# Performance work log

Measured on AMD Instinct MI355X. Metric: run time of the kernel, lower is better.

## Reference

```python
import jax, jax.numpy as jnp
import numpy as np


def _compact_positions(mask, K):
    """mask: [B, T] bool. Returns [B, K] with the (ascending) indices t where
    mask[b, t] is True, compacted to the front; remaining slots are -1.
    Stable argsort on ~mask puts True positions first, preserving order.
    """
    order = jnp.argsort(jnp.logical_not(mask), axis=1, stable=True)  # [B, T]
    counts = mask.sum(axis=1, keepdims=True)                          # [B, 1]
    pos = order[:, :K]                                                # [B, K]
    valid = jnp.arange(K)[None, :] < jnp.minimum(counts, K)
    return jnp.where(valid, pos, -1)


def setup_inputs() -> dict:
    key = jax.random.key(0)
    k_r, k_e = jax.random.split(key)
    B, MAX_ROUTING, D = 16, 4096, 512
    routing = jax.random.randint(k_r, (B, MAX_ROUTING), 0, 2, dtype=jnp.int32)
    pos_embed = jax.random.normal(k_e, (MAX_ROUTING, D), dtype=jnp.float32)
    return {"routing": routing, "max_nodes": 1024, "max_edges": 2048,
            "pos_embed": pos_embed}


def reference(routing, max_nodes, max_edges, pos_embed):
    # Compacted logical positions of node tokens (routing==0) and edge tokens
    # (routing==1), replacing the sequential per-batch Python loop.
    node_pos = _compact_positions(routing == 0, max_nodes)  # [B, max_nodes]
    edge_pos = _compact_positions(routing == 1, max_edges)  # [B, max_edges]

    # Each node spans 2 tokens, each edge spans 5 tokens:
    # unsqueeze(-1).repeat(...,k).view == elementwise repeat along axis 1.
    node_tok = jnp.repeat(node_pos, 2, axis=1)  # [B, max_nodes*2]
    edge_tok = jnp.repeat(edge_pos, 5, axis=1)  # [B, max_edges*5]

    node_pe = pos_embed[jnp.maximum(node_tok, 0)]  # [B, max_nodes*2, D]
    edge_pe = pos_embed[jnp.maximum(edge_tok, 0)]  # [B, max_edges*5, D]
    return node_pe, edge_pe
```

## Files before the change

kernel.cpp:

```cpp
#include <hip/hip_runtime.h>

#define NB 16
#define NT 4096
#define ND 512
#define ND4 128
#define MAX_NODES 1024
#define MAX_EDGES 2048
#define NODE_ROWS 2048
#define EDGE_ROWS 10240

__global__ __launch_bounds__(1024) void compact_kernel(
    const int* __restrict__ routing,
    int* __restrict__ node_pos,
    int* __restrict__ edge_pos)
{
    const int b   = blockIdx.x;
    const int tid = threadIdx.x;
    const int lane = tid & 63;
    const int wv   = tid >> 6;

    const int4 v = reinterpret_cast<const int4*>(routing + b * NT)[tid];
    const int e0 = v.x, e1 = v.y, e2 = v.z, e3 = v.w;

    unsigned inc0 = ((e0 == 0) ? 0x10000u : 0u) | ((e0 == 1) ? 1u : 0u);
    unsigned inc1 = ((e1 == 0) ? 0x10000u : 0u) | ((e1 == 1) ? 1u : 0u);
    unsigned inc2 = ((e2 == 0) ? 0x10000u : 0u) | ((e2 == 1) ? 1u : 0u);
    unsigned inc3 = ((e3 == 0) ? 0x10000u : 0u) | ((e3 == 1) ? 1u : 0u);
    unsigned p0 = inc0;
    unsigned p1 = p0 + inc1;
    unsigned p2 = p1 + inc2;
    unsigned p3 = p2 + inc3;
    const unsigned my_sum = p3;

    unsigned x = my_sum;
    #pragma unroll
    for (int off = 1; off < 64; off <<= 1) {
        unsigned y = __shfl_up(x, off, 64);
        if (lane >= off) x += y;
    }

    __shared__ unsigned wave_sums[16];
    if (lane == 63) wave_sums[wv] = x;

    node_pos[b * MAX_NODES + tid] = -1;
    edge_pos[b * MAX_EDGES + 2 * tid + 0] = -1;
    edge_pos[b * MAX_EDGES + 2 * tid + 1] = -1;
    __syncthreads();

    unsigned offset = 0;
    for (int i = 0; i < wv; ++i) offset += wave_sums[i];

    const unsigned base = offset + x - my_sum;

    const unsigned ex0 = base;
    const unsigned ex1 = base + p0;
    const unsigned ex2 = base + p1;
    const unsigned ex3 = base + p2;

    const int t0 = tid * 4;
    #pragma unroll 4
    for (int i = 0; i < 4; ++i) {
        const int      e  = (i == 0) ? e0 : (i == 1) ? e1 : (i == 2) ? e2 : e3;
        const unsigned ex = (i == 0) ? ex0 : (i == 1) ? ex1 : (i == 2) ? ex2 : ex3;
        if (e == 0) {
            const unsigned rank = ex >> 16;
            if (rank < MAX_NODES) node_pos[b * MAX_NODES + rank] = t0 + i;
        } else if (e == 1) {
            const unsigned rank = ex & 0xFFFFu;
            if (rank < MAX_EDGES) edge_pos[b * MAX_EDGES + rank] = t0 + i;
        }
    }
}

__global__ __launch_bounds__(256) void gather_node_kernel(
    const float4* __restrict__ pe,
    const int* __restrict__ node_pos,
    float4* __restrict__ out)
{
    const unsigned gid = blockIdx.x * 256u + threadIdx.x;
    const unsigned row = gid >> 7;
    const unsigned c   = gid & 127u;
    const unsigned b   = row >> 11;
    const unsigned j   = row & 2047u;
    const int tok = node_pos[b * MAX_NODES + (j >> 1)];
    const int src = tok < 0 ? 0 : tok;
    out[(size_t)row * ND4 + c] = pe[(size_t)src * ND4 + c];
}

__global__ __launch_bounds__(256) void gather_edge_kernel(
    const float4* __restrict__ pe,
    const int* __restrict__ edge_pos,
    float4* __restrict__ out)
{
    const unsigned gid = blockIdx.x * 256u + threadIdx.x;
    const unsigned row = gid >> 7;
    const unsigned c   = gid & 127u;
    const unsigned b   = row / EDGE_ROWS;
    const unsigned j   = row - b * EDGE_ROWS;
    const int tok = edge_pos[b * MAX_EDGES + j / 5u];
    const int src = tok < 0 ? 0 : tok;
    out[(size_t)row * ND4 + c] = pe[(size_t)src * ND4 + c];
}

extern "C" void kernel_launch(void* const* d_in, const int* in_sizes, int n_in,
                              void* d_out, int out_size, void* d_ws, size_t ws_size,
                              hipStream_t stream) {
    const int*   routing = (const int*)d_in[0];
    const float* pe      = (const float*)d_in[3];

    int* node_pos = (int*)d_ws;
    int* edge_pos = node_pos + NB * MAX_NODES;

    float* out_node = (float*)d_out;
    float* out_edge = out_node + (size_t)NB * NODE_ROWS * ND;

    compact_kernel<<<NB, 1024, 0, stream>>>(routing, node_pos, edge_pos);

    const unsigned node_threads = NB * NODE_ROWS * ND4;
    const unsigned edge_threads = NB * EDGE_ROWS * ND4;
    gather_node_kernel<<<node_threads / 256, 256, 0, stream>>>(
        (const float4*)pe, node_pos, (float4*)out_node);
    gather_edge_kernel<<<edge_threads / 256, 256, 0, stream>>>(
        (const float4*)pe, edge_pos, (float4*)out_edge);
}
```

Measured before the change: 428.5 us.

## Fuse node and edge gathers into one kernel with nontemporal stores

Merges the two gather kernels into a single launch covering all output rows, assigning 64 threads per row with each thread copying two float4s. Output writes use nontemporal stores so the large streaming output does not pollute cache. The intent is to remove one kernel launch and its tail, halve the index loads per row, and improve write streaming. The cost is a per-thread branch between the node and edge paths.

```diff
diff --git a/kernel.cpp b/kernel.cpp
--- a/kernel.cpp
+++ b/kernel.cpp
@@ -8,6 +8,10 @@
 #define MAX_EDGES 2048
 #define NODE_ROWS 2048
 #define EDGE_ROWS 10240
+#define ROWS_NODE_TOT 32768u
+#define ROWS_TOTAL 196608u
+
+typedef __attribute__((ext_vector_type(4))) float f4;
 
 __global__ __launch_bounds__(1024) void compact_kernel(
     const int* __restrict__ routing,
@@ -72,34 +76,36 @@
     }
 }
 
-__global__ __launch_bounds__(256) void gather_node_kernel(
+__global__ __launch_bounds__(256) void gather_fused_kernel(
     const float4* __restrict__ pe,
     const int* __restrict__ node_pos,
-    float4* __restrict__ out)
-{
-    const unsigned gid = blockIdx.x * 256u + threadIdx.x;
-    const unsigned row = gid >> 7;
-    const unsigned c   = gid & 127u;
-    const unsigned b   = row >> 11;
-    const unsigned j   = row & 2047u;
-    const int tok = node_pos[b * MAX_NODES + (j >> 1)];
-    const int src = tok < 0 ? 0 : tok;
-    out[(size_t)row * ND4 + c] = pe[(size_t)src * ND4 + c];
-}
-
-__global__ __launch_bounds__(256) void gather_edge_kernel(
-    const float4* __restrict__ pe,
     const int* __restrict__ edge_pos,
     float4* __restrict__ out)
 {
     const unsigned gid = blockIdx.x * 256u + threadIdx.x;
-    const unsigned row = gid >> 7;
-    const unsigned c   = gid & 127u;
-    const unsigned b   = row / EDGE_ROWS;
-    const unsigned j   = row - b * EDGE_ROWS;
-    const int tok = edge_pos[b * MAX_EDGES + j / 5u];
+    const unsigned row = gid >> 6;
+    const unsigned t   = gid & 63u;
+
+    int tok;
+    if (row < ROWS_NODE_TOT) {
+        const unsigned b = row >> 11;
+        const unsigned j = row & 2047u;
+        tok = node_pos[b * MAX_NODES + (j >> 1)];
+    } else {
+        const unsigned r2 = row - ROWS_NODE_TOT;
+        const unsigned b  = r2 / EDGE_ROWS;
+        const unsigned j  = r2 - b * EDGE_ROWS;
+        tok = edge_pos[b * MAX_EDGES + j / 5u];
+    }
     const int src = tok < 0 ? 0 : tok;
-    out[(size_t)row * ND4 + c] = pe[(size_t)src * ND4 + c];
+
+    const f4* srcp = (const f4*)(pe + (size_t)src * ND4);
+    f4* dstp       = (f4*)(out + (size_t)row * ND4);
+
+    const f4 v0 = srcp[t];
+    const f4 v1 = srcp[t + 64];
+    __builtin_nontemporal_store(v0, dstp + t);
+    __builtin_nontemporal_store(v1, dstp + t + 64);
 }
 
 extern "C" void kernel_launch(void* const* d_in, const int* in_sizes, int n_in,
@@ -111,15 +117,9 @@
     int* node_pos = (int*)d_ws;
     int* edge_pos = node_pos + NB * MAX_NODES;
 
-    float* out_node = (float*)d_out;
-    float* out_edge = out_node + (size_t)NB * NODE_ROWS * ND;
-
     compact_kernel<<<NB, 1024, 0, stream>>>(routing, node_pos, edge_pos);
 
-    const unsigned node_threads = NB * NODE_ROWS * ND4;
-    const unsigned edge_threads = NB * EDGE_ROWS * ND4;
-    gather_node_kernel<<<node_threads / 256, 256, 0, stream>>>(
-        (const float4*)pe, node_pos, (float4*)out_node);
-    gather_edge_kernel<<<edge_threads / 256, 256, 0, stream>>>(
-        (const float4*)pe, edge_pos, (float4*)out_edge);
+    const unsigned total_threads = ROWS_TOTAL * 64u;
+    gather_fused_kernel<<<total_threads / 256, 256, 0, stream>>>(
+        (const float4*)pe, node_pos, edge_pos, (float4*)d_out);
 }
```

After: 404.2 us. 5.7% less time.
